# Kernel tuning notes

Measured on AMD Instinct MI355X. Metric: run time of the kernel, lower is better.

Reference implementation:

```python
import jax, jax.numpy as jnp
import numpy as np

H_DIM = 1024
N_HEADS = 16
HEAD_D = H_DIM // N_HEADS  # 64


def setup_inputs() -> dict:
    key = jax.random.key(0)
    ks = jax.random.split(key, 10)
    B, T, C = 2, 2048, H_DIM
    init = 1.0 / np.sqrt(C)  # lecun_normal-scale stand-in
    src = jax.random.normal(ks[0], (B, T, C), dtype=jnp.float32)
    mask = jnp.ones((B, T), dtype=jnp.float32)  # unused when causal
    Wq = jax.random.normal(ks[1], (C, H_DIM), dtype=jnp.float32) * init
    Wk = jax.random.normal(ks[2], (C, H_DIM), dtype=jnp.float32) * init
    Wv = jax.random.normal(ks[3], (C, H_DIM), dtype=jnp.float32) * init
    Wo = jax.random.normal(ks[4], (H_DIM, H_DIM), dtype=jnp.float32) * init
    bq = jnp.zeros((H_DIM,), jnp.float32)
    bk = jnp.zeros((H_DIM,), jnp.float32)
    bv = jnp.zeros((H_DIM,), jnp.float32)
    bo = jnp.zeros((H_DIM,), jnp.float32)
    return {"src": src, "mask": mask, "Wq": Wq, "bq": bq, "Wk": Wk, "bk": bk,
            "Wv": Wv, "bv": bv, "Wo": Wo, "bo": bo}


def reference(src, mask, Wq, bq, Wk, bk, Wv, bv, Wo, bo):
    # MaskedCausalAttention forward, deterministic=True (dropout = identity),
    # use_causal_mask=True.
    B, T, C = src.shape
    N, D = N_HEADS, HEAD_D
    # q,k,v: [B, N, T, D]
    q = (src @ Wq + bq).reshape(B, T, N, D).transpose(0, 2, 1, 3)
    k = (src @ Wk + bk).reshape(B, T, N, D).transpose(0, 2, 1, 3)
    v = (src @ Wv + bv).reshape(B, T, N, D).transpose(0, 2, 1, 3)
    # scores: [B, N, T, T]
    scores = jnp.einsum('bntd,bnsd->bnts', q, k) / jnp.sqrt(jnp.float32(D))
    causal = jnp.tril(jnp.ones((T, T), dtype=bool))[None, None]
    scores = jnp.where(causal, scores, -jnp.inf)
    probs = jax.nn.softmax(scores, axis=-1)
    attn = jnp.einsum('bnts,bnsd->bntd', probs, v)  # [B, N, T, D]
    attn = attn.transpose(0, 2, 1, 3).reshape(B, T, N * D)
    return attn @ Wo + bo
```

## Files before the change

kernel.cpp:

```cpp
#include <hip/hip_runtime.h>
#include <hip/hip_bf16.h>

typedef __hip_bfloat16 bf16;
typedef __attribute__((ext_vector_type(8))) short short8;
typedef __attribute__((ext_vector_type(4))) float f32x4;

#define BATCH 2
#define SEQ   2048
#define HDIM  1024
#define NHEAD 16
#define DHEAD 64
#define MROWS (BATCH*SEQ)

#define QSCALE 0.18033688f
#define EXP2F(x) __builtin_amdgcn_exp2f(x)

static __device__ __forceinline__ short f2bs(float x) {
    __hip_bfloat16 h = (__hip_bfloat16)x;
    return *reinterpret_cast<short*>(&h);
}
static __device__ __forceinline__ unsigned int pk2(float a, float b) {
    __hip_bfloat162 h = __float22bfloat162_rn(make_float2(a, b));
    return *reinterpret_cast<unsigned int*>(&h);
}

static __device__ __forceinline__ void gload16(const void* g, void* l) {
    __builtin_amdgcn_global_load_lds(
        (const __attribute__((address_space(1))) unsigned int*)g,
        (__attribute__((address_space(3))) unsigned int*)l, 16, 0, 0);
}

__global__ __launch_bounds__(256) void prep1(const float* __restrict__ src,
        const float* __restrict__ Wq, const float* __restrict__ Wk,
        const float* __restrict__ Wv, const float* __restrict__ Wo,
        short* __restrict__ Sb, short* __restrict__ WT,
        short* __restrict__ WoT)
{
    __shared__ float t[64][65];
    const int bx = blockIdx.x, tid = threadIdx.x;
    if (bx < 4096) {
        int i = bx * 256 + tid;
        float4 v = ((const float4*)src)[i];
        ushort4 o;
        o.x = (unsigned short)f2bs(v.x);
        o.y = (unsigned short)f2bs(v.y);
        o.z = (unsigned short)f2bs(v.z);
        o.w = (unsigned short)f2bs(v.w);
        ((ushort4*)Sb)[i] = o;
        return;
    }
    const int tb = bx - 4096;
    const int wsel = tb >> 8;
    const float* W = (wsel == 0) ? Wq : (wsel == 1) ? Wk : (wsel == 2) ? Wv : Wo;
    short* dst = (wsel < 3) ? WT : WoT;
    const int roff = (wsel < 3) ? wsel * 1024 : 0;
    const int t8 = tb & 255;
    const int n0 = (t8 & 15) * 64, k0 = (t8 >> 4) * 64;
#pragma unroll
    for (int i = 0; i < 16; i++) {
        int idx = tid + i * 256, r = idx >> 6, c = idx & 63;
        t[r][c] = W[(size_t)(k0 + r) * HDIM + n0 + c];
    }
    __syncthreads();
#pragma unroll
    for (int i = 0; i < 16; i++) {
        int idx = tid + i * 256, c = idx >> 6, r = idx & 63;
        dst[(size_t)(roff + n0 + c) * HDIM + k0 + r] = f2bs(t[r][c]);
    }
}

__global__ __launch_bounds__(512, 2) void gemm_qkv(const short* __restrict__ A,
        const short* __restrict__ Bt,
        const float* __restrict__ bq, const float* __restrict__ bk,
        const float* __restrict__ bv,
        short* __restrict__ Qout, short* __restrict__ Kout,
        short* __restrict__ Vtout)
{
    __shared__ short SM[2][32768];
    const int tid = threadIdx.x, lane = tid & 63, w = tid >> 6;
    const int quad = lane >> 4, l15 = lane & 15;
    const int m0 = blockIdx.y * 256, n0 = blockIdx.x * 256;
    const int wr = w >> 1, wc = w & 1;

    const short* gp[4][2];
    int lo[4][2];
#pragma unroll
    for (int g = 0; g < 4; g++)
#pragma unroll
        for (int i = 0; i < 2; i++) {
            if (g < 2) {
                int u = g * 16 + w * 2 + i;
                gp[g][i] = A + (size_t)(m0 + (u >> 1) * 16 + l15) * HDIM
                             + (u & 1) * 32 + quad * 8;
                lo[g][i] = u * 512;
            } else {
                int j = w * 2 + i;
                int v = (g == 2 ? 0 : 8) + j + (j >= 8 ? 8 : 0);
                gp[g][i] = Bt + (size_t)(n0 + (v >> 1) * 16 + l15) * HDIM
                              + (v & 1) * 32 + quad * 8;
                lo[g][i] = 16384 + v * 512;
            }
        }

    f32x4 acc[4][8];
#pragma unroll
    for (int i = 0; i < 4; i++)
#pragma unroll
        for (int j = 0; j < 8; j++) acc[i][j] = (f32x4){0.f, 0.f, 0.f, 0.f};

#pragma unroll
    for (int g = 0; g < 4; g++)
#pragma unroll
        for (int i = 0; i < 2; i++) { gload16(gp[g][i], &SM[0][lo[g][i]]); gp[g][i] += 64; }
    asm volatile("s_waitcnt vmcnt(2)" ::: "memory");
    __builtin_amdgcn_s_barrier();

    short8 af[4][2];
    for (int t = 0; t < 16; ++t) {
        const short* Tb = SM[t & 1];
        short* Sn = SM[(t + 1) & 1];
#pragma unroll
        for (int p = 0; p < 4; ++p) {
            if (p == 0) {
#pragma unroll
                for (int mi = 0; mi < 4; mi++)
#pragma unroll
                    for (int kh = 0; kh < 2; kh++)
                        af[mi][kh] = *(const short8*)
                            &Tb[((wr * 4 + mi) * 2 + kh) * 512 + lane * 8];
            }
            short8 bfp[2][2];
#pragma unroll
            for (int n2 = 0; n2 < 2; n2++)
#pragma unroll
                for (int kh = 0; kh < 2; kh++)
                    bfp[n2][kh] = *(const short8*)
                        &Tb[16384 + ((wc * 8 + p * 2 + n2) * 2 + kh) * 512 + lane * 8];

            if (t < 15) {
                gload16(gp[p][0], Sn + lo[p][0]); gp[p][0] += 64;
                gload16(gp[p][1], Sn + lo[p][1]); gp[p][1] += 64;
                if (p == 1) asm volatile("s_waitcnt vmcnt(4)" ::: "memory");
                if (p == 3) asm volatile("s_waitcnt vmcnt(2)" ::: "memory");
            } else {
                if (p == 1) asm volatile("s_waitcnt vmcnt(0)" ::: "memory");
            }
            __builtin_amdgcn_s_barrier();
            __builtin_amdgcn_s_setprio(1);
#pragma unroll
            for (int n2 = 0; n2 < 2; n2++)
#pragma unroll
                for (int mi = 0; mi < 4; mi++)
#pragma unroll
                    for (int kh = 0; kh < 2; kh++)
                        acc[mi][p * 2 + n2] = __builtin_amdgcn_mfma_f32_16x16x32_bf16(
                            af[mi][kh], bfp[n2][kh], acc[mi][p * 2 + n2], 0, 0, 0);
            __builtin_amdgcn_s_setprio(0);
            __builtin_amdgcn_s_barrier();
        }
    }

    const int region = blockIdx.x >> 2;
    if (region < 2) {
        const float* bias = region ? bk : bq;
        const float oscale = region ? 1.0f : QSCALE;
        short* C = region ? Kout : Qout;
#pragma unroll
        for (int mi = 0; mi < 4; mi++) {
            int mB = m0 + wr * 64 + mi * 16 + quad * 4;
#pragma unroll
            for (int ni = 0; ni < 8; ni++) {
                int nl = (n0 + (wc * 8 + ni) * 16 + l15) & 1023;
                float bb = bias[nl];
#pragma unroll
                for (int r = 0; r < 4; r++)
                    C[(size_t)(mB + r) * HDIM + nl] =
                        f2bs((acc[mi][ni][r] + bb) * oscale);
            }
        }
    } else {
#pragma unroll
        for (int mi = 0; mi < 4; mi++) {
            int mB = m0 + wr * 64 + mi * 16 + quad * 4;
            int bb = mB >> 11, tt = mB & 2047;
#pragma unroll
            for (int ni = 0; ni < 8; ni++) {
                int n = n0 + (wc * 8 + ni) * 16 + l15;
                int h = (n >> 6) & 15, d = n & 63;
                float bvv = bv[n & 1023];
                size_t base = ((size_t)((bb * NHEAD + h) * DHEAD + d)) * SEQ + tt;
                ushort4 pk;
                pk.x = (unsigned short)f2bs(acc[mi][ni][0] + bvv);
                pk.y = (unsigned short)f2bs(acc[mi][ni][1] + bvv);
                pk.z = (unsigned short)f2bs(acc[mi][ni][2] + bvv);
                pk.w = (unsigned short)f2bs(acc[mi][ni][3] + bvv);
                *(ushort4*)(Vtout + base) = pk;
            }
        }
    }
}

__global__ __launch_bounds__(256) void attn_mfma(const short* __restrict__ Qb,
        const short* __restrict__ Kb, const short* __restrict__ Vt,
        short* __restrict__ Ab,
        float* __restrict__ Opart, float* __restrict__ Psum)
{
    __shared__ short SMEM[20992];
    const int tid = threadIdx.x, lane = tid & 63, w = tid >> 6;
    const int quad = lane >> 4, l15 = lane & 15;
    const int L = blockIdx.x;

    const int pair = (L & 7) + 8 * ((L >> 3) & 3);
    const int u = L >> 5;
    const int b = pair >> 4, head = pair & 15;
    int s, it0, itEnd, half, split;
    if (u < 32) {
        split = 1; s = 31 - (u >> 1); half = u & 1;
        int mid = (s + 2) >> 1;
        it0 = half ? mid : 0;
        itEnd = half ? (s + 1) : mid;
    } else {
        split = 0; s = 47 - u; half = 0; it0 = 0; itEnd = s + 1;
    }
    const int nj = itEnd - it0;

    const short* Kbh = Kb + (size_t)b * SEQ * HDIM + head * DHEAD;
    const short* Vth = Vt + (size_t)(b * NHEAD + head) * DHEAD * SEQ;
    short* Pw = SMEM + 16384 + w * 1152;

    const int qr = s * 64 + w * 16 + l15;

    const short* qptr = Qb + (size_t)(b * SEQ + qr) * HDIM + head * DHEAD + quad * 8;
    short8 bq0 = *(const short8*)qptr;
    short8 bq1 = *(const short8*)(qptr + 32);

    const short* gp[4];
    int stp[4], ldo[4];
#pragma unroll
    for (int i = 0; i < 4; i++) {
        int c8 = w * 4 + i;
        if (c8 < 8) {
            int t = c8 >> 1, h = c8 & 1;
            gp[i] = Kbh + (size_t)(t * 16 + l15) * HDIM + h * 32 + quad * 8;
            stp[i] = 64 * HDIM;
        } else {
            int c = c8 - 8, dt = c >> 1, kh = c & 1;
            gp[i] = Vth + (size_t)(dt * 16 + l15) * SEQ + kh * 32 + quad * 8;
            stp[i] = 64;
        }
        ldo[i] = c8 * 512;
        gp[i] += (size_t)it0 * stp[i];
    }

    f32x4 o[4];
#pragma unroll
    for (int dt = 0; dt < 4; dt++) o[dt] = (f32x4){0.f, 0.f, 0.f, 0.f};
    float psum = 0.f;

#pragma unroll
    for (int i = 0; i < 4; i++) { gload16(gp[i], &SMEM[ldo[i]]); gp[i] += stp[i]; }

    for (int j = 0; j < nj; ++j) {
        const int cur = j & 1;
        short* Ks = &SMEM[cur * 8192];
        short* Vs = Ks + 4096;

        if (j + 1 < nj) {
            short* nb = &SMEM[(cur ^ 1) * 8192];
#pragma unroll
            for (int i = 0; i < 4; i++) { gload16(gp[i], nb + ldo[i]); gp[i] += stp[i]; }
            asm volatile("s_waitcnt vmcnt(4)" ::: "memory");
        } else {
            asm volatile("s_waitcnt vmcnt(0)" ::: "memory");
        }
        __builtin_amdgcn_s_barrier();
        const int itg = it0 + j;
        const int s0 = itg * 64;
        f32x4 sv[4];
        __builtin_amdgcn_s_setprio(1);
#pragma unroll
        for (int t = 0; t < 4; t++) {
            sv[t] = (f32x4){0.f, 0.f, 0.f, 0.f};
            short8 k0 = *(const short8*)&Ks[(t * 2) * 512 + lane * 8];
            short8 k1 = *(const short8*)&Ks[(t * 2 + 1) * 512 + lane * 8];
            sv[t] = __builtin_amdgcn_mfma_f32_16x16x32_bf16(k0, bq0, sv[t], 0, 0, 0);
            sv[t] = __builtin_amdgcn_mfma_f32_16x16x32_bf16(k1, bq1, sv[t], 0, 0, 0);
        }
        __builtin_amdgcn_s_setprio(0);

        float p[16];
        if (itg == s) {
#pragma unroll
            for (int t = 0; t < 4; t++)
#pragma unroll
                for (int r = 0; r < 4; r++) {
                    int key = s0 + t * 16 + quad * 4 + r;
                    p[t * 4 + r] = (key <= qr) ? EXP2F(sv[t][r]) : 0.f;
                }
        } else {
#pragma unroll
            for (int t = 0; t < 4; t++)
#pragma unroll
                for (int r = 0; r < 4; r++)
                    p[t * 4 + r] = EXP2F(sv[t][r]);
        }
#pragma unroll
        for (int i = 0; i < 16; i++) psum += p[i];

#pragma unroll
        for (int t = 0; t < 4; t++) {
            uint2 u2;
            u2.x = pk2(p[t * 4],     p[t * 4 + 1]);
            u2.y = pk2(p[t * 4 + 2], p[t * 4 + 3]);
            *(uint2*)&Pw[l15 * 72 + t * 16 + quad * 4] = u2;
        }
        short8 bp0 = *(const short8*)&Pw[l15 * 72 + quad * 8];
        short8 bp1 = *(const short8*)&Pw[l15 * 72 + 32 + quad * 8];

        __builtin_amdgcn_s_setprio(1);
#pragma unroll
        for (int dt = 0; dt < 4; dt++) {
            short8 av0 = *(const short8*)&Vs[(dt * 2) * 512 + lane * 8];
            short8 av1 = *(const short8*)&Vs[(dt * 2 + 1) * 512 + lane * 8];
            o[dt] = __builtin_amdgcn_mfma_f32_16x16x32_bf16(av0, bp0, o[dt], 0, 0, 0);
            o[dt] = __builtin_amdgcn_mfma_f32_16x16x32_bf16(av1, bp1, o[dt], 0, 0, 0);
        }
        __builtin_amdgcn_s_setprio(0);
        __builtin_amdgcn_s_barrier();
    }

    float lrow = psum + __shfl_xor(psum, 16);
    lrow += __shfl_xor(lrow, 32);

    if (split) {
        const int tile = (pair * 16 + (s - 16)) * 2 + half;
        float* Ot = Opart + (size_t)tile * 4096;
        const int rho = w * 16 + l15;
#pragma unroll
        for (int dt = 0; dt < 4; dt++)
            *(f32x4*)&Ot[rho * 64 + dt * 16 + quad * 4] = o[dt];
        if (quad == 0) Psum[tile * 64 + rho] = lrow;
        return;
    }

    const float inv = 1.f / lrow;
    const size_t obase = (size_t)(b * SEQ + qr) * HDIM + head * DHEAD;
#pragma unroll
    for (int dt = 0; dt < 4; dt++) {
        uint2 u2;
        u2.x = pk2(o[dt][0] * inv, o[dt][1] * inv);
        u2.y = pk2(o[dt][2] * inv, o[dt][3] * inv);
        *(uint2*)&Ab[obase + dt * 16 + quad * 4] = u2;
    }
}

__global__ __launch_bounds__(256) void combine(const float* __restrict__ Opart,
        const float* __restrict__ Psum, short* __restrict__ Ab)
{
    const int bxx = blockIdx.x;
    const int pair = bxx & 31, sidx = bxx >> 5;
    const int b = pair >> 4, head = pair & 15;
    const int s = 16 + sidx;
    const int tid = threadIdx.x;
    const int row = tid >> 2, dq = (tid & 3) * 16;

    const size_t t0 = ((size_t)(pair * 16 + sidx) * 2) * 4096;
    const float* O0 = Opart + t0;
    const float* O1 = O0 + 4096;
    const int p0 = (pair * 16 + sidx) * 2 * 64;
    const float inv = 1.f / (Psum[p0 + row] + Psum[p0 + 64 + row]);

    const size_t obase = (size_t)(b * SEQ + s * 64 + row) * HDIM + head * DHEAD + dq;
#pragma unroll
    for (int g = 0; g < 4; g++) {
        float4 a = *(const float4*)&O0[row * 64 + dq + g * 4];
        float4 c = *(const float4*)&O1[row * 64 + dq + g * 4];
        ushort4 pk;
        pk.x = (unsigned short)f2bs((a.x + c.x) * inv);
        pk.y = (unsigned short)f2bs((a.y + c.y) * inv);
        pk.z = (unsigned short)f2bs((a.z + c.z) * inv);
        pk.w = (unsigned short)f2bs((a.w + c.w) * inv);
        *(ushort4*)&Ab[obase + g * 4] = pk;
    }
}

__global__ __launch_bounds__(512) void gemm_o(const short* __restrict__ A,
        const short* __restrict__ Bt, const float* __restrict__ bo,
        float* __restrict__ Out)
{
    __shared__ short SM[2 * 16384];
    const int tid = threadIdx.x, lane = tid & 63, w = tid >> 6;
    const int quad = lane >> 4, l15 = lane & 15;
    const int m0 = blockIdx.y * 128, n0 = blockIdx.x * 128;
    const int wr = w >> 2, wc = w & 3;

    const short* gsrc[4];
    short* ldst[4];
#pragma unroll
    for (int i = 0; i < 4; i++) {
        int c8 = w * 4 + i;
        if (c8 < 16) {
            gsrc[i] = A + (size_t)(m0 + (c8 >> 1) * 16 + l15) * HDIM
                        + (c8 & 1) * 32 + quad * 8;
            ldst[i] = &SM[c8 * 512];
        } else {
            int v = c8 - 16;
            gsrc[i] = Bt + (size_t)(n0 + (v >> 1) * 16 + l15) * HDIM
                         + (v & 1) * 32 + quad * 8;
            ldst[i] = &SM[8192 + v * 512];
        }
    }

    f32x4 acc[4][2];
#pragma unroll
    for (int i = 0; i < 4; i++)
#pragma unroll
        for (int j = 0; j < 2; j++) acc[i][j] = (f32x4){0.f, 0.f, 0.f, 0.f};

#pragma unroll
    for (int i = 0; i < 4; i++) { gload16(gsrc[i], ldst[i]); gsrc[i] += 64; }

    for (int kk = 0; kk < 16; ++kk) {
        const int cur = kk & 1;
        if (kk < 15) {
            const int nb = (cur ^ 1) * 16384;
#pragma unroll
            for (int i = 0; i < 4; i++) { gload16(gsrc[i], ldst[i] + nb); gsrc[i] += 64; }
            asm volatile("s_waitcnt vmcnt(4)" ::: "memory");
        } else {
            asm volatile("s_waitcnt vmcnt(0)" ::: "memory");
        }
        __builtin_amdgcn_s_barrier();

        const short* Asb = &SM[cur * 16384];
        const short* Bsb = Asb + 8192;
#pragma unroll
        for (int kh = 0; kh < 2; kh++) {
            short8 af[4], bfr[2];
#pragma unroll
            for (int mi = 0; mi < 4; mi++)
                af[mi] = *(const short8*)&Asb[((wr * 4 + mi) * 2 + kh) * 512 + lane * 8];
#pragma unroll
            for (int ni = 0; ni < 2; ni++)
                bfr[ni] = *(const short8*)&Bsb[((wc * 2 + ni) * 2 + kh) * 512 + lane * 8];
#pragma unroll
            for (int mi = 0; mi < 4; mi++)
#pragma unroll
                for (int ni = 0; ni < 2; ni++)
                    acc[mi][ni] = __builtin_amdgcn_mfma_f32_16x16x32_bf16(
                                      af[mi], bfr[ni], acc[mi][ni], 0, 0, 0);
        }
        __builtin_amdgcn_s_barrier();
    }

#pragma unroll
    for (int mi = 0; mi < 4; mi++) {
        int mB = m0 + (wr * 4 + mi) * 16 + quad * 4;
#pragma unroll
        for (int ni = 0; ni < 2; ni++) {
            int n = n0 + (wc * 2 + ni) * 16 + l15;
            float bb = bo[n];
#pragma unroll
            for (int r = 0; r < 4; r++)
                Out[(size_t)(mB + r) * HDIM + n] = acc[mi][ni][r] + bb;
        }
    }
}

extern "C" void kernel_launch(void* const* d_in, const int* in_sizes, int n_in,
                              void* d_out, int out_size, void* d_ws, size_t ws_size,
                              hipStream_t stream)
{
    const float* src = (const float*)d_in[0];
    const float* Wq = (const float*)d_in[2];
    const float* bq = (const float*)d_in[3];
    const float* Wk = (const float*)d_in[4];
    const float* bk = (const float*)d_in[5];
    const float* Wv = (const float*)d_in[6];
    const float* bv = (const float*)d_in[7];
    const float* Wo = (const float*)d_in[8];
    const float* bo = (const float*)d_in[9];
    float* out = (float*)d_out;

    short* Sb   = (short*)d_ws;
    short* Qb   = Sb + (size_t)MROWS * HDIM;
    short* Kb   = Qb + (size_t)MROWS * HDIM;
    short* Vt   = Kb + (size_t)MROWS * HDIM;
    short* WoT  = Vt + (size_t)MROWS * HDIM;
    short* WT   = (short*)d_out;
    short* Ab   = Qb;
    float* Opart = (float*)d_out;
    float* Psum  = (float*)Sb;

    prep1<<<dim3(4096 + 1024), dim3(256), 0, stream>>>(src, Wq, Wk, Wv, Wo, Sb, WT, WoT);

    gemm_qkv<<<dim3(12, 16), dim3(512), 0, stream>>>(Sb, WT, bq, bk, bv, Qb, Kb, Vt);

    attn_mfma<<<dim3(1536), dim3(256), 0, stream>>>(Qb, Kb, Vt, Ab, Opart, Psum);

    combine<<<dim3(512), dim3(256), 0, stream>>>(Opart, Psum, Ab);

    gemm_o<<<dim3(8, 32), dim3(512), 0, stream>>>(Ab, WoT, bo, out);
}
```

Measured before the change: 203.8 us.

## Restructure QKV GEMM main loop into two halves with one barrier per k-step

Replaces the four-phase inner loop of the projection GEMM, which synchronised twice per phase, with one barrier at the top of each k-step. After that barrier the wave reads all A fragments and the first half of the B fragments, issues every global-to-LDS prefetch for the next tile, and runs the first MFMA block. It then waits on vmcnt and runs the second half. The aim is to cut barrier and wait overhead and give the prefetches more compute to hide behind. The catch is that the second-half B reads rely only on a per-wave vmcnt wait with no barrier. Data written to LDS by other waves may therefore not be visible yet, which risks a race, and the change also raises register pressure.

```diff
diff --git a/kernel.cpp b/kernel.cpp
--- a/kernel.cpp
+++ b/kernel.cpp
@@ -112,52 +112,67 @@
     for (int g = 0; g < 4; g++)
 #pragma unroll
         for (int i = 0; i < 2; i++) { gload16(gp[g][i], &SM[0][lo[g][i]]); gp[g][i] += 64; }
-    asm volatile("s_waitcnt vmcnt(2)" ::: "memory");
-    __builtin_amdgcn_s_barrier();
 
     short8 af[4][2];
     for (int t = 0; t < 16; ++t) {
         const short* Tb = SM[t & 1];
         short* Sn = SM[(t + 1) & 1];
-#pragma unroll
-        for (int p = 0; p < 4; ++p) {
-            if (p == 0) {
-#pragma unroll
-                for (int mi = 0; mi < 4; mi++)
-#pragma unroll
-                    for (int kh = 0; kh < 2; kh++)
-                        af[mi][kh] = *(const short8*)
-                            &Tb[((wr * 4 + mi) * 2 + kh) * 512 + lane * 8];
-            }
-            short8 bfp[2][2];
-#pragma unroll
-            for (int n2 = 0; n2 < 2; n2++)
+
+        asm volatile("s_waitcnt vmcnt(2)" ::: "memory");
+        __builtin_amdgcn_s_barrier();
+#pragma unroll
+        for (int mi = 0; mi < 4; mi++)
+#pragma unroll
+            for (int kh = 0; kh < 2; kh++)
+                af[mi][kh] = *(const short8*)
+                    &Tb[((wr * 4 + mi) * 2 + kh) * 512 + lane * 8];
+        short8 bf01[4][2];
+#pragma unroll
+        for (int nn = 0; nn < 4; nn++)
+#pragma unroll
+            for (int kh = 0; kh < 2; kh++)
+                bf01[nn][kh] = *(const short8*)
+                    &Tb[16384 + ((wc * 8 + nn) * 2 + kh) * 512 + lane * 8];
+
+        if (t < 15) {
+#pragma unroll
+            for (int g = 0; g < 4; g++)
+#pragma unroll
+                for (int i = 0; i < 2; i++) { gload16(gp[g][i], Sn + lo[g][i]); gp[g][i] += 64; }
+        }
+
+        __builtin_amdgcn_s_setprio(1);
+#pragma unroll
+        for (int nn = 0; nn < 4; nn++)
+#pragma unroll
+            for (int mi = 0; mi < 4; mi++)
 #pragma unroll
                 for (int kh = 0; kh < 2; kh++)
-                    bfp[n2][kh] = *(const short8*)
-                        &Tb[16384 + ((wc * 8 + p * 2 + n2) * 2 + kh) * 512 + lane * 8];
-
-            if (t < 15) {
-                gload16(gp[p][0], Sn + lo[p][0]); gp[p][0] += 64;
-                gload16(gp[p][1], Sn + lo[p][1]); gp[p][1] += 64;
-                if (p == 1) asm volatile("s_waitcnt vmcnt(4)" ::: "memory");
-                if (p == 3) asm volatile("s_waitcnt vmcnt(2)" ::: "memory");
-            } else {
-                if (p == 1) asm volatile("s_waitcnt vmcnt(0)" ::: "memory");
-            }
-            __builtin_amdgcn_s_barrier();
-            __builtin_amdgcn_s_setprio(1);
-#pragma unroll
-            for (int n2 = 0; n2 < 2; n2++)
-#pragma unroll
-                for (int mi = 0; mi < 4; mi++)
-#pragma unroll
-                    for (int kh = 0; kh < 2; kh++)
-                        acc[mi][p * 2 + n2] = __builtin_amdgcn_mfma_f32_16x16x32_bf16(
-                            af[mi][kh], bfp[n2][kh], acc[mi][p * 2 + n2], 0, 0, 0);
-            __builtin_amdgcn_s_setprio(0);
-            __builtin_amdgcn_s_barrier();
-        }
+                    acc[mi][nn] = __builtin_amdgcn_mfma_f32_16x16x32_bf16(
+                        af[mi][kh], bf01[nn][kh], acc[mi][nn], 0, 0, 0);
+        __builtin_amdgcn_s_setprio(0);
+
+        if (t < 15) asm volatile("s_waitcnt vmcnt(8)" ::: "memory");
+        else        asm volatile("s_waitcnt vmcnt(0)" ::: "memory");
+
+        short8 bf23[4][2];
+#pragma unroll
+        for (int nn = 0; nn < 4; nn++)
+#pragma unroll
+            for (int kh = 0; kh < 2; kh++)
+                bf23[nn][kh] = *(const short8*)
+                    &Tb[16384 + ((wc * 8 + 4 + nn) * 2 + kh) * 512 + lane * 8];
+
+        __builtin_amdgcn_s_setprio(1);
+#pragma unroll
+        for (int nn = 0; nn < 4; nn++)
+#pragma unroll
+            for (int mi = 0; mi < 4; mi++)
+#pragma unroll
+                for (int kh = 0; kh < 2; kh++)
+                    acc[mi][4 + nn] = __builtin_amdgcn_mfma_f32_16x16x32_bf16(
+                        af[mi][kh], bf23[nn][kh], acc[mi][4 + nn], 0, 0, 0);
+        __builtin_amdgcn_s_setprio(0);
     }
 
     const int region = blockIdx.x >> 2;
@@ -274,6 +289,7 @@
             asm volatile("s_waitcnt vmcnt(0)" ::: "memory");
         }
         __builtin_amdgcn_s_barrier();
+
         const int itg = it0 + j;
         const int s0 = itg * 64;
         f32x4 sv[4];
```

After: 204.5 us. No clear change (+0.4%).

## Retile QKV GEMM to 256x192 tiles and simplify its pipeline

Applied to the files above, without the earlier changes.

The QKV projection GEMM tile narrows from 256x256 to 256x192, so the grid grows from 12x16=192 blocks to 16x16=256, which matches the MI355X CU count more closely. The K-loop's four sub-phases, each with its own barrier, become one wait, one barrier, a bulk fragment load and a full MFMA burst per K step. Because a 192-wide tile can straddle the Q/K/V boundary, the epilogue now picks the output region per 16-column fragment. Waiting on vmcnt(0) before each step shrinks the overlap between prefetch and compute, and shared memory still holds two buffers.

```diff
diff --git a/kernel.cpp b/kernel.cpp
--- a/kernel.cpp
+++ b/kernel.cpp
@@ -76,118 +76,98 @@
         short* __restrict__ Qout, short* __restrict__ Kout,
         short* __restrict__ Vtout)
 {
-    __shared__ short SM[2][32768];
+    __shared__ short SM[2][28672];
     const int tid = threadIdx.x, lane = tid & 63, w = tid >> 6;
     const int quad = lane >> 4, l15 = lane & 15;
-    const int m0 = blockIdx.y * 256, n0 = blockIdx.x * 256;
+    const int m0 = blockIdx.y * 256, n0 = blockIdx.x * 192;
     const int wr = w >> 1, wc = w & 1;
 
-    const short* gp[4][2];
-    int lo[4][2];
-#pragma unroll
-    for (int g = 0; g < 4; g++)
-#pragma unroll
-        for (int i = 0; i < 2; i++) {
-            if (g < 2) {
-                int u = g * 16 + w * 2 + i;
-                gp[g][i] = A + (size_t)(m0 + (u >> 1) * 16 + l15) * HDIM
-                             + (u & 1) * 32 + quad * 8;
-                lo[g][i] = u * 512;
-            } else {
-                int j = w * 2 + i;
-                int v = (g == 2 ? 0 : 8) + j + (j >= 8 ? 8 : 0);
-                gp[g][i] = Bt + (size_t)(n0 + (v >> 1) * 16 + l15) * HDIM
-                              + (v & 1) * 32 + quad * 8;
-                lo[g][i] = 16384 + v * 512;
-            }
-        }
-
-    f32x4 acc[4][8];
+    const short* gp[7];
+    int lo[7];
+#pragma unroll
+    for (int i = 0; i < 7; i++) {
+        int c = w * 7 + i;
+        if (c < 32) {
+            gp[i] = A + (size_t)(m0 + (c >> 1) * 16 + l15) * HDIM
+                      + (c & 1) * 32 + quad * 8;
+            lo[i] = c * 512;
+        } else {
+            int v = c - 32;
+            gp[i] = Bt + (size_t)(n0 + (v >> 1) * 16 + l15) * HDIM
+                       + (v & 1) * 32 + quad * 8;
+            lo[i] = 16384 + v * 512;
+        }
+    }
+
+    f32x4 acc[4][6];
 #pragma unroll
     for (int i = 0; i < 4; i++)
 #pragma unroll
-        for (int j = 0; j < 8; j++) acc[i][j] = (f32x4){0.f, 0.f, 0.f, 0.f};
-
-#pragma unroll
-    for (int g = 0; g < 4; g++)
-#pragma unroll
-        for (int i = 0; i < 2; i++) { gload16(gp[g][i], &SM[0][lo[g][i]]); gp[g][i] += 64; }
-    asm volatile("s_waitcnt vmcnt(2)" ::: "memory");
-    __builtin_amdgcn_s_barrier();
-
-    short8 af[4][2];
+        for (int j = 0; j < 6; j++) acc[i][j] = (f32x4){0.f, 0.f, 0.f, 0.f};
+
+#pragma unroll
+    for (int i = 0; i < 7; i++) { gload16(gp[i], &SM[0][lo[i]]); gp[i] += 64; }
+
     for (int t = 0; t < 16; ++t) {
         const short* Tb = SM[t & 1];
         short* Sn = SM[(t + 1) & 1];
-#pragma unroll
-        for (int p = 0; p < 4; ++p) {
-            if (p == 0) {
-#pragma unroll
-                for (int mi = 0; mi < 4; mi++)
-#pragma unroll
-                    for (int kh = 0; kh < 2; kh++)
-                        af[mi][kh] = *(const short8*)
-                            &Tb[((wr * 4 + mi) * 2 + kh) * 512 + lane * 8];
-            }
-            short8 bfp[2][2];
-#pragma unroll
-            for (int n2 = 0; n2 < 2; n2++)
+
+        asm volatile("s_waitcnt vmcnt(0)" ::: "memory");
+        __builtin_amdgcn_s_barrier();
+        short8 af[4][2], bf[6][2];
+#pragma unroll
+        for (int mi = 0; mi < 4; mi++)
+#pragma unroll
+            for (int kh = 0; kh < 2; kh++)
+                af[mi][kh] = *(const short8*)
+                    &Tb[((wr * 4 + mi) * 2 + kh) * 512 + lane * 8];
+#pragma unroll
+        for (int nn = 0; nn < 6; nn++)
+#pragma unroll
+            for (int kh = 0; kh < 2; kh++)
+                bf[nn][kh] = *(const short8*)
+                    &Tb[16384 + ((wc * 6 + nn) * 2 + kh) * 512 + lane * 8];
+
+        if (t < 15) {
+#pragma unroll
+            for (int i = 0; i < 7; i++) { gload16(gp[i], Sn + lo[i]); gp[i] += 64; }
+        }
+
+        __builtin_amdgcn_s_setprio(1);
+#pragma unroll
+        for (int nn = 0; nn < 6; nn++)
+#pragma unroll
+            for (int mi = 0; mi < 4; mi++)
 #pragma unroll
                 for (int kh = 0; kh < 2; kh++)
-                    bfp[n2][kh] = *(const short8*)
-                        &Tb[16384 + ((wc * 8 + p * 2 + n2) * 2 + kh) * 512 + lane * 8];
-
-            if (t < 15) {
-                gload16(gp[p][0], Sn + lo[p][0]); gp[p][0] += 64;
-                gload16(gp[p][1], Sn + lo[p][1]); gp[p][1] += 64;
-                if (p == 1) asm volatile("s_waitcnt vmcnt(4)" ::: "memory");
-                if (p == 3) asm volatile("s_waitcnt vmcnt(2)" ::: "memory");
+                    acc[mi][nn] = __builtin_amdgcn_mfma_f32_16x16x32_bf16(
+                        af[mi][kh], bf[nn][kh], acc[mi][nn], 0, 0, 0);
+        __builtin_amdgcn_s_setprio(0);
+    }
+
+#pragma unroll
+    for (int mi = 0; mi < 4; mi++) {
+        int mB = m0 + wr * 64 + mi * 16 + quad * 4;
+        int bb = mB >> 11, tt = mB & 2047;
+#pragma unroll
+        for (int ni = 0; ni < 6; ni++) {
+            int n = n0 + wc * 96 + ni * 16 + l15;
+            int rg = n >> 10, nl = n & 1023;
+            if (rg == 0) {
+                float bbv = bq[nl];
+#pragma unroll
+                for (int r = 0; r < 4; r++)
+                    Qout[(size_t)(mB + r) * HDIM + nl] =
+                        f2bs((acc[mi][ni][r] + bbv) * QSCALE);
+            } else if (rg == 1) {
+                float bbv = bk[nl];
+#pragma unroll
+                for (int r = 0; r < 4; r++)
+                    Kout[(size_t)(mB + r) * HDIM + nl] =
+                        f2bs(acc[mi][ni][r] + bbv);
             } else {
-                if (p == 1) asm volatile("s_waitcnt vmcnt(0)" ::: "memory");
-            }
-            __builtin_amdgcn_s_barrier();
-            __builtin_amdgcn_s_setprio(1);
-#pragma unroll
-            for (int n2 = 0; n2 < 2; n2++)
-#pragma unroll
-                for (int mi = 0; mi < 4; mi++)
-#pragma unroll
-                    for (int kh = 0; kh < 2; kh++)
-                        acc[mi][p * 2 + n2] = __builtin_amdgcn_mfma_f32_16x16x32_bf16(
-                            af[mi][kh], bfp[n2][kh], acc[mi][p * 2 + n2], 0, 0, 0);
-            __builtin_amdgcn_s_setprio(0);
-            __builtin_amdgcn_s_barrier();
-        }
-    }
-
-    const int region = blockIdx.x >> 2;
-    if (region < 2) {
-        const float* bias = region ? bk : bq;
-        const float oscale = region ? 1.0f : QSCALE;
-        short* C = region ? Kout : Qout;
-#pragma unroll
-        for (int mi = 0; mi < 4; mi++) {
-            int mB = m0 + wr * 64 + mi * 16 + quad * 4;
-#pragma unroll
-            for (int ni = 0; ni < 8; ni++) {
-                int nl = (n0 + (wc * 8 + ni) * 16 + l15) & 1023;
-                float bb = bias[nl];
-#pragma unroll
-                for (int r = 0; r < 4; r++)
-                    C[(size_t)(mB + r) * HDIM + nl] =
-                        f2bs((acc[mi][ni][r] + bb) * oscale);
-            }
-        }
-    } else {
-#pragma unroll
-        for (int mi = 0; mi < 4; mi++) {
-            int mB = m0 + wr * 64 + mi * 16 + quad * 4;
-            int bb = mB >> 11, tt = mB & 2047;
-#pragma unroll
-            for (int ni = 0; ni < 8; ni++) {
-                int n = n0 + (wc * 8 + ni) * 16 + l15;
-                int h = (n >> 6) & 15, d = n & 63;
-                float bvv = bv[n & 1023];
+                float bvv = bv[nl];
+                int h = nl >> 6, d = nl & 63;
                 size_t base = ((size_t)((bb * NHEAD + h) * DHEAD + d)) * SEQ + tt;
                 ushort4 pk;
                 pk.x = (unsigned short)f2bs(acc[mi][ni][0] + bvv);
@@ -274,6 +254,7 @@
             asm volatile("s_waitcnt vmcnt(0)" ::: "memory");
         }
         __builtin_amdgcn_s_barrier();
+
         const int itg = it0 + j;
         const int s0 = itg * 64;
         f32x4 sv[4];
@@ -494,7 +475,7 @@
 
     prep1<<<dim3(4096 + 1024), dim3(256), 0, stream>>>(src, Wq, Wk, Wv, Wo, Sb, WT, WoT);
 
-    gemm_qkv<<<dim3(12, 16), dim3(512), 0, stream>>>(Sb, WT, bq, bk, bv, Qb, Kb, Vt);
+    gemm_qkv<<<dim3(16, 16), dim3(512), 0, stream>>>(Sb, WT, bq, bk, bv, Qb, Kb, Vt);
 
     attn_mfma<<<dim3(1536), dim3(256), 0, stream>>>(Qb, Kb, Vt, Ab, Opart, Psum);
 
```

New measurement: 204.3 us. Within noise of the previous version (+0.2%).
